# Kernel optimization log

Measured on AMD Instinct MI355X. Metric: run time of the kernel, lower is better.

The kernel has to match this reference:

```python
import jax, jax.numpy as jnp
import numpy as np

B, H, W, C, NH = 4, 128, 128, 192, 6
KD = C // NH          # key/head dim = 32
SCALING = KD ** -0.5


def dwconv5x5(v, kernel, bias):
    # v: (b,h,w,c), depthwise 5x5, stride 1, pad 2. kernel: (5,5,1,c)
    out = jax.lax.conv_general_dilated(
        v, kernel, window_strides=(1, 1), padding=[(2, 2), (2, 2)],
        dimension_numbers=("NHWC", "HWIO", "NHWC"), feature_group_count=C)
    return out + bias


def setup_inputs() -> dict:
    key = jax.random.key(0)
    ks = jax.random.split(key, 13)
    s = C ** -0.5
    return {
        "x": jax.random.normal(ks[0], (B, H, W, C), jnp.float32),
        "mask_h": 0.1 * jax.random.normal(ks[1], (1, NH, H, H), jnp.float32),
        "mask_w": 0.1 * jax.random.normal(ks[2], (1, NH, W, W), jnp.float32),
        "Wq": s * jax.random.normal(ks[3], (C, C), jnp.float32),
        "bq": 0.01 * jax.random.normal(ks[4], (C,), jnp.float32),
        "Wk": s * jax.random.normal(ks[5], (C, C), jnp.float32),
        "bk": 0.01 * jax.random.normal(ks[6], (C,), jnp.float32),
        "Wv": s * jax.random.normal(ks[7], (C, C), jnp.float32),
        "bv": 0.01 * jax.random.normal(ks[8], (C,), jnp.float32),
        "lepe_w": 0.05 * jax.random.normal(ks[9], (5, 5, 1, C), jnp.float32),
        "lepe_b": jnp.zeros((C,), jnp.float32),
        "Wo": s * jax.random.normal(ks[10], (C, C), jnp.float32),
        "bo": jnp.zeros((C,), jnp.float32),
    }


def reference(x, mask_h, mask_w, Wq, bq, Wk, bk, Wv, bv, lepe_w, lepe_b, Wo, bo):
    b, h, w, _ = x.shape
    q = x @ Wq + bq                                   # (b,h,w,c)
    k = (x @ Wk + bk) * SCALING
    v = x @ Wv + bv
    lepe = dwconv5x5(v, lepe_w, lepe_b)               # (b,h,w,c)

    qr = q.reshape(b, h, w, NH, KD)                   # (b,h,w,n,k)
    kr = k.reshape(b, h, w, NH, KD)
    vr = v.reshape(b, h, w, NH, KD)                   # head_dim == KD (factor=1)

    # ---- row (width-axis) attention ----
    # scores: (b,h,n,w,w')
    qk_w = jnp.einsum("bhwnk,bhunk->bhnwu", qr, kr)
    qk_w = qk_w + mask_w[:, None]                     # (1,1,n,w,w) broadcast over h
    attn_w = jax.nn.softmax(qk_w, axis=-1)
    v1 = jnp.einsum("bhnwu,bhund->bhnwd", attn_w, vr)  # (b,h,n,w,d)

    # ---- column (height-axis) attention ----
    # scores: (b,w,n,h,h')
    qk_h = jnp.einsum("bhwnk,bjwnk->bwnhj", qr, kr)
    qk_h = qk_h + mask_h[:, None]                     # (1,1,n,h,h) broadcast over w
    attn_h = jax.nn.softmax(qk_h, axis=-1)
    out = jnp.einsum("bwnhj,bjnwd->bhwnd", attn_h, v1)  # (b,h,w,n,d)

    out = out.reshape(b, h, w, C) + lepe
    return out @ Wo + bo
```

## Files before the change

### kernel.cpp

```cpp
#include <hip/hip_runtime.h>
#include <hip/hip_bf16.h>

#define BB  4
#define HH  128
#define WW  128
#define CC  192
#define NHH 6
#define KDD 32
#define NTOT (BB*HH*WW*CC)
#define SCALING 0.17677669529663687f
#define WMAT_ELE (12*6*64*8)

typedef __hip_bfloat16 bf16;
typedef short bf16x8 __attribute__((ext_vector_type(8)));
typedef unsigned short ushortx4 __attribute__((ext_vector_type(4)));
typedef float floatx4 __attribute__((ext_vector_type(4)));

__device__ __forceinline__ float b2f(bf16 v) { return __bfloat162float(v); }
__device__ __forceinline__ bf16  f2b(float v) { return __float2bfloat16(v); }
__device__ __forceinline__ unsigned short f2bs(float f) {
  union { bf16 b; unsigned short u; } c; c.b = __float2bfloat16(f); return c.u;
}
__device__ __forceinline__ float s2f(short s) {
  union { unsigned u; float f; } c;
  c.u = ((unsigned)(unsigned short)s) << 16; return c.f;
}

__global__ __launch_bounds__(256) void prep_kernel(
    const float* __restrict__ Wq, const float* __restrict__ Wk,
    const float* __restrict__ Wv, const float* __restrict__ Wo,
    unsigned short* __restrict__ Wt) {
  const int idx = blockIdx.x * 256 + threadIdx.x;
  if (idx >= 4 * 12 * 6 * 64) return;
  const int lane = idx & 63;
  int rest = idx >> 6;
  const int kc = rest % 6; rest /= 6;
  const int nt = rest % 12;
  const int mat = rest / 12;
  const int r16 = lane & 15, quad = lane >> 4;
  const float* W = (mat == 0) ? Wq : (mat == 1) ? Wk : (mat == 2) ? Wv : Wo;
  const float sc = (mat == 1) ? SCALING : 1.f;
  bf16x8 t;
  #pragma unroll
  for (int j = 0; j < 8; ++j)
    t[j] = (short)f2bs(W[(kc * 32 + quad * 8 + j) * CC + nt * 16 + r16] * sc);
  *reinterpret_cast<bf16x8*>(&Wt[(size_t)idx * 8]) = t;
}

__global__ __launch_bounds__(256) void qkv_mfma(
    const float* __restrict__ x, const unsigned short* __restrict__ Wt,
    const float* __restrict__ bq, const float* __restrict__ bk,
    const float* __restrict__ bv,
    bf16* __restrict__ q, bf16* __restrict__ k, bf16* __restrict__ v) {
  __shared__ __align__(16) unsigned short Wlds[18432];
  const int tid = threadIdx.x;
  const int l = tid & 63;
  const int r16 = l & 15, quad = l >> 4;
  const int row0 = blockIdx.x * 64 + (tid >> 6) * 16;
  const floatx4 zero = {0.f, 0.f, 0.f, 0.f};
  bf16x8 a[6];
  {
    const float* xrow = x + (row0 + r16) * CC;
    #pragma unroll
    for (int kc = 0; kc < 6; ++kc) {
      const float4* p = reinterpret_cast<const float4*>(xrow + kc * 32 + quad * 8);
      float4 u0 = p[0], u1 = p[1];
      bf16x8 t;
      t[0]=f2bs(u0.x); t[1]=f2bs(u0.y); t[2]=f2bs(u0.z); t[3]=f2bs(u0.w);
      t[4]=f2bs(u1.x); t[5]=f2bs(u1.y); t[6]=f2bs(u1.z); t[7]=f2bs(u1.w);
      a[kc] = t;
    }
  }
  for (int mat = 0; mat < 3; ++mat) {
    const unsigned short* Wm = Wt + mat * WMAT_ELE;
    bf16* outp = (mat == 0) ? q : (mat == 1) ? k : v;
    const float* bias = (mat == 0) ? bq : (mat == 1) ? bk : bv;
    const float bscale = (mat == 1) ? SCALING : 1.f;
    for (int hf = 0; hf < 2; ++hf) {
      __syncthreads();
      #pragma unroll
      for (int c = 0; c < 9; ++c) {
        const int ci = c * 256 + tid;
        *reinterpret_cast<bf16x8*>(&Wlds[ci * 8]) =
            *reinterpret_cast<const bf16x8*>(&Wm[hf * 18432 + ci * 8]);
      }
      __syncthreads();
      #pragma unroll
      for (int ntl = 0; ntl < 6; ++ntl) {
        const int nt = hf * 6 + ntl;
        bf16x8 wfr[6];
        #pragma unroll
        for (int kc = 0; kc < 6; ++kc)
          wfr[kc] = *reinterpret_cast<const bf16x8*>(
              &Wlds[((ntl * 6 + kc) * 64 + l) * 8]);
        floatx4 acc = zero;
        #pragma unroll
        for (int kc = 0; kc < 6; ++kc)
          acc = __builtin_amdgcn_mfma_f32_16x16x32_bf16(wfr[kc], a[kc], acc, 0, 0, 0);
        const int col0 = nt * 16 + quad * 4;
        const float4 b4 = *reinterpret_cast<const float4*>(bias + col0);
        ushortx4 s0;
        s0[0] = f2bs(acc[0] + b4.x * bscale);
        s0[1] = f2bs(acc[1] + b4.y * bscale);
        s0[2] = f2bs(acc[2] + b4.z * bscale);
        s0[3] = f2bs(acc[3] + b4.w * bscale);
        *reinterpret_cast<ushortx4*>(&outp[(row0 + r16) * CC + col0]) = s0;
      }
    }
  }
}

__global__ __launch_bounds__(256) void lepe_kernel(
    const bf16* __restrict__ v, const float* __restrict__ kw,
    const float* __restrict__ kb, float* __restrict__ lepe) {
  __shared__ __align__(16) unsigned short patch[12 * 132 * 8];
  const int tid = threadIdx.x;
  const int bid = blockIdx.x;
  const int x8 = bid & 7;
  const int kk = bid >> 3;
  const int cg = kk % 24;
  const int tile = (kk / 24) * 8 + x8;
  const int hb = tile & 15;
  const int b  = tile >> 4;
  const int c0 = cg * 8;
  const int h0 = hb * 8;
  const bf16x8 vzero = {0, 0, 0, 0, 0, 0, 0, 0};
  for (int i = tid; i < 12 * 132; i += 256) {
    const int row = i / 132, col = i % 132;
    const int gh = h0 + row - 2, gw = col - 2;
    bf16x8 t = vzero;
    if ((unsigned)gh < HH && (unsigned)gw < WW)
      t = *reinterpret_cast<const bf16x8*>(
          v + ((b * HH + gh) * WW + gw) * CC + c0);
    *reinterpret_cast<bf16x8*>(&patch[i * 8]) = t;
  }
  __syncthreads();
  const int wo = tid & 127;
  const int r0 = (tid >> 7) * 4;
  float acc[4][8];
  {
    const float4* kbp = reinterpret_cast<const float4*>(kb + c0);
    float4 b0 = kbp[0], b1 = kbp[1];
    #pragma unroll
    for (int j = 0; j < 4; ++j) {
      acc[j][0]=b0.x; acc[j][1]=b0.y; acc[j][2]=b0.z; acc[j][3]=b0.w;
      acc[j][4]=b1.x; acc[j][5]=b1.y; acc[j][6]=b1.z; acc[j][7]=b1.w;
    }
  }
  const unsigned short* pbase = &patch[(r0 * 132 + wo) * 8];
  for (int kh = 0; kh < 5; ++kh) {
    #pragma unroll
    for (int kwi = 0; kwi < 5; ++kwi) {
      const float4* kp = reinterpret_cast<const float4*>(
          kw + (kh * 5 + kwi) * CC + c0);
      float4 k0 = kp[0], k1 = kp[1];
      #pragma unroll
      for (int j = 0; j < 4; ++j) {
        bf16x8 t = *reinterpret_cast<const bf16x8*>(
            pbase + ((j + kh) * 132 + kwi) * 8);
        acc[j][0] = fmaf(s2f(t[0]), k0.x, acc[j][0]);
        acc[j][1] = fmaf(s2f(t[1]), k0.y, acc[j][1]);
        acc[j][2] = fmaf(s2f(t[2]), k0.z, acc[j][2]);
        acc[j][3] = fmaf(s2f(t[3]), k0.w, acc[j][3]);
        acc[j][4] = fmaf(s2f(t[4]), k1.x, acc[j][4]);
        acc[j][5] = fmaf(s2f(t[5]), k1.y, acc[j][5]);
        acc[j][6] = fmaf(s2f(t[6]), k1.z, acc[j][6]);
        acc[j][7] = fmaf(s2f(t[7]), k1.w, acc[j][7]);
      }
    }
  }
  #pragma unroll
  for (int j = 0; j < 4; ++j) {
    float4* op = reinterpret_cast<float4*>(
        lepe + ((b * HH + h0 + r0 + j) * WW + wo) * CC + c0);
    op[0] = make_float4(acc[j][0], acc[j][1], acc[j][2], acc[j][3]);
    op[1] = make_float4(acc[j][4], acc[j][5], acc[j][6], acc[j][7]);
  }
}

__global__ __launch_bounds__(256) void attn_mfma_kernel(
    const bf16* __restrict__ qg, const bf16* __restrict__ kg,
    bf16* vbuf, const float* __restrict__ mask,
    const float* __restrict__ lepeadd, const int rstride, const int is_col) {
  __shared__ __align__(16) unsigned short Kf[8 * 64 * 8];
  __shared__ __align__(16) unsigned short Vf[8 * 64 * 8];
  __shared__ unsigned short P[4 * 16 * 136];
  const int bid = blockIdx.x;
  const int x8 = bid & 7;
  const int kk = bid >> 3;
  const int n = kk % NHH;
  const int g = x8 * 64 + kk / NHH;
  const int p = g & 127, b = g >> 7;
  const int base = is_col ? ((b * HH * WW + p) * CC + n * KDD)
                          : (((b * HH + p) * WW) * CC + n * KDD);
  const int tid = threadIdx.x;
  const int l = tid & 63, w = tid >> 6;
  const int r16 = l & 15, quad = l >> 4;
  const float* mbase = mask + n * 128 * 128;
  const floatx4 zero = {0.f, 0.f, 0.f, 0.f};
  const unsigned short* vg = (const unsigned short*)vbuf;

  #pragma unroll
  for (int c = 0; c < 2; ++c) {
    const int chunk = c * 256 + tid;
    const int key = chunk >> 2, q4 = chunk & 3;
    const int gaddr = base + key * rstride + q4 * 8;
    bf16x8 tk = *reinterpret_cast<const bf16x8*>(kg + gaddr);
    bf16x8 tv = *reinterpret_cast<const bf16x8*>(vg + gaddr);
    *reinterpret_cast<bf16x8*>(
        &Kf[(((key >> 4) * 4 + q4) * 16 + (key & 15)) * 8]) = tk;
    const int s = key >> 5, hi = (key >> 3) & 3, j = key & 7;
    #pragma unroll
    for (int m = 0; m < 8; ++m) {
      const int ch = q4 * 8 + m;
      const int nj = ch >> 4, rr = ch & 15;
      Vf[((s * 2 + nj) * 64 + hi * 16 + rr) * 8 + j] = (unsigned short)tv[m];
    }
  }
  __syncthreads();

  unsigned short* Pw = &P[w * 2176];
  #pragma unroll
  for (int t2 = 0; t2 < 2; ++t2) {
    const int mi = w * 2 + t2;
    bf16x8 qf = *reinterpret_cast<const bf16x8*>(
        qg + base + (mi * 16 + r16) * rstride + quad * 8);
    floatx4 S[8];
    #pragma unroll
    for (int ni = 0; ni < 8; ++ni) {
      bf16x8 kfr = *reinterpret_cast<const bf16x8*>(&Kf[(ni * 64 + l) * 8]);
      S[ni] = __builtin_amdgcn_mfma_f32_16x16x32_bf16(qf, kfr, zero, 0, 0, 0);
    }
    #pragma unroll
    for (int ni = 0; ni < 8; ++ni)
      #pragma unroll
      for (int i = 0; i < 4; ++i)
        S[ni][i] += mbase[(mi * 16 + quad * 4 + i) * 128 + ni * 16 + r16];
    float linv[4], mrow[4];
    #pragma unroll
    for (int i = 0; i < 4; ++i) {
      float m = S[0][i];
      #pragma unroll
      for (int ni = 1; ni < 8; ++ni) m = fmaxf(m, S[ni][i]);
      m = fmaxf(m, __shfl_xor(m, 1));
      m = fmaxf(m, __shfl_xor(m, 2));
      m = fmaxf(m, __shfl_xor(m, 4));
      m = fmaxf(m, __shfl_xor(m, 8));
      mrow[i] = m;
    }
    #pragma unroll
    for (int i = 0; i < 4; ++i) {
      float lsum = 0.f;
      #pragma unroll
      for (int ni = 0; ni < 8; ++ni) {
        const float pv = __expf(S[ni][i] - mrow[i]);
        S[ni][i] = pv;
        lsum += pv;
      }
      lsum += __shfl_xor(lsum, 1);
      lsum += __shfl_xor(lsum, 2);
      lsum += __shfl_xor(lsum, 4);
      lsum += __shfl_xor(lsum, 8);
      linv[i] = 1.f / lsum;
    }
    #pragma unroll
    for (int ni = 0; ni < 8; ++ni)
      #pragma unroll
      for (int i = 0; i < 4; ++i)
        Pw[(quad * 4 + i) * 136 + ni * 16 + r16] = f2bs(S[ni][i] * linv[i]);
    floatx4 O[2] = {zero, zero};
    #pragma unroll
    for (int s = 0; s < 4; ++s) {
      bf16x8 pf = *reinterpret_cast<const bf16x8*>(
          &Pw[r16 * 136 + s * 32 + quad * 8]);
      #pragma unroll
      for (int nj = 0; nj < 2; ++nj) {
        bf16x8 vfr = *reinterpret_cast<const bf16x8*>(
            &Vf[((s * 2 + nj) * 64 + l) * 8]);
        O[nj] = __builtin_amdgcn_mfma_f32_16x16x32_bf16(pf, vfr, O[nj], 0, 0, 0);
      }
    }
    #pragma unroll
    for (int nj = 0; nj < 2; ++nj)
      #pragma unroll
      for (int i = 0; i < 4; ++i) {
        const int addr = base + (mi * 16 + quad * 4 + i) * rstride + nj * 16 + r16;
        float val = O[nj][i];
        if (lepeadd) val += lepeadd[addr];
        vbuf[addr] = f2b(val);
      }
  }
}

__global__ __launch_bounds__(256) void proj_mfma(
    const bf16* __restrict__ pre, const unsigned short* __restrict__ Wto,
    const float* __restrict__ bo, float* __restrict__ out) {
  __shared__ __align__(16) unsigned short Wlds[18432];
  const int tid = threadIdx.x;
  const int l = tid & 63;
  const int r16 = l & 15, quad = l >> 4;
  const int row0 = blockIdx.x * 128 + (tid >> 6) * 32;
  const floatx4 zero = {0.f, 0.f, 0.f, 0.f};
  bf16x8 a[2][6];
  #pragma unroll
  for (int rs = 0; rs < 2; ++rs)
    #pragma unroll
    for (int kc = 0; kc < 6; ++kc)
      a[rs][kc] = *reinterpret_cast<const bf16x8*>(
          pre + (row0 + rs * 16 + r16) * CC + kc * 32 + quad * 8);
  for (int hf = 0; hf < 2; ++hf) {
    __syncthreads();
    #pragma unroll
    for (int c = 0; c < 9; ++c) {
      const int ci = c * 256 + tid;
      *reinterpret_cast<bf16x8*>(&Wlds[ci * 8]) =
          *reinterpret_cast<const bf16x8*>(&Wto[hf * 18432 + ci * 8]);
    }
    __syncthreads();
    #pragma unroll
    for (int ntl = 0; ntl < 6; ++ntl) {
      const int nt = hf * 6 + ntl;
      bf16x8 wfr[6];
      #pragma unroll
      for (int kc = 0; kc < 6; ++kc)
        wfr[kc] = *reinterpret_cast<const bf16x8*>(
            &Wlds[((ntl * 6 + kc) * 64 + l) * 8]);
      floatx4 acc0 = zero, acc1 = zero;
      #pragma unroll
      for (int kc = 0; kc < 6; ++kc) {
        acc0 = __builtin_amdgcn_mfma_f32_16x16x32_bf16(wfr[kc], a[0][kc], acc0, 0, 0, 0);
        acc1 = __builtin_amdgcn_mfma_f32_16x16x32_bf16(wfr[kc], a[1][kc], acc1, 0, 0, 0);
      }
      const int col0 = nt * 16 + quad * 4;
      const float4 b4 = *reinterpret_cast<const float4*>(bo + col0);
      float4 s0 = make_float4(acc0[0] + b4.x, acc0[1] + b4.y,
                              acc0[2] + b4.z, acc0[3] + b4.w);
      float4 s1 = make_float4(acc1[0] + b4.x, acc1[1] + b4.y,
                              acc1[2] + b4.z, acc1[3] + b4.w);
      *reinterpret_cast<float4*>(&out[(row0 + r16) * CC + col0]) = s0;
      *reinterpret_cast<float4*>(&out[(row0 + 16 + r16) * CC + col0]) = s1;
    }
  }
}

extern "C" void kernel_launch(void* const* d_in, const int* in_sizes, int n_in,
                              void* d_out, int out_size, void* d_ws, size_t ws_size,
                              hipStream_t stream) {
  const float* x      = (const float*)d_in[0];
  const float* mask_h = (const float*)d_in[1];
  const float* mask_w = (const float*)d_in[2];
  const float* Wq = (const float*)d_in[3];
  const float* bq = (const float*)d_in[4];
  const float* Wk = (const float*)d_in[5];
  const float* bk = (const float*)d_in[6];
  const float* Wv = (const float*)d_in[7];
  const float* bv = (const float*)d_in[8];
  const float* lw = (const float*)d_in[9];
  const float* lb = (const float*)d_in[10];
  const float* Wo = (const float*)d_in[11];
  const float* bo = (const float*)d_in[12];
  float* out = (float*)d_out;

  bf16* q    = (bf16*)d_ws;
  bf16* kbuf = q + NTOT;
  bf16* v    = kbuf + NTOT;
  unsigned short* Wt = (unsigned short*)(v + NTOT);

  prep_kernel<<<(4*12*6*64 + 255)/256, 256, 0, stream>>>(Wq, Wk, Wv, Wo, Wt);
  qkv_mfma<<<(BB*HH*WW)/64, 256, 0, stream>>>(x, Wt, bq, bk, bv, q, kbuf, v);
  lepe_kernel<<<BB*16*24, 256, 0, stream>>>(v, lw, lb, out);
  attn_mfma_kernel<<<BB*128*NHH, 256, 0, stream>>>(
      q, kbuf, v, mask_w, nullptr, CC, 0);
  attn_mfma_kernel<<<BB*128*NHH, 256, 0, stream>>>(
      q, kbuf, v, mask_h, out, WW*CC, 1);
  proj_mfma<<<(BB*HH*WW)/128, 256, 0, stream>>>(v, Wt + 3*WMAT_ELE, bo, out);
}
```

Before: 276.4 us.

## Double-buffer QKV weight staging with async global-to-LDS loads

The QKV projection kernel now stages weight tiles through two LDS buffers using direct global_load_lds instructions, prefetching the next quarter-matrix while computing the current one. Weight phases are split into 12 smaller chunks instead of 6 halves, so LDS use stays the same but the load no longer passes through registers or sits on the critical path. This depends on the async LDS load finishing before the __syncthreads barrier without an explicit vmcnt wait, which is a correctness risk. The QKV kernel is only part of the total pipeline time.

```diff
diff --git a/kernel.cpp b/kernel.cpp
--- a/kernel.cpp
+++ b/kernel.cpp
@@ -24,6 +24,13 @@
 __device__ __forceinline__ float s2f(short s) {
   union { unsigned u; float f; } c;
   c.u = ((unsigned)(unsigned short)s) << 16; return c.f;
+}
+
+__device__ __forceinline__ void stage16(const unsigned short* g,
+                                        unsigned short* l) {
+  __builtin_amdgcn_global_load_lds(
+      (const __attribute__((address_space(1))) void*)g,
+      (__attribute__((address_space(3))) void*)l, 16, 0, 0);
 }
 
 __global__ __launch_bounds__(256) void prep_kernel(
@@ -52,11 +59,11 @@
     const float* __restrict__ bq, const float* __restrict__ bk,
     const float* __restrict__ bv,
     bf16* __restrict__ q, bf16* __restrict__ k, bf16* __restrict__ v) {
-  __shared__ __align__(16) unsigned short Wlds[18432];
+  __shared__ __align__(16) unsigned short Wlds[2][9216];
   const int tid = threadIdx.x;
-  const int l = tid & 63;
+  const int l = tid & 63, w = tid >> 6;
   const int r16 = l & 15, quad = l >> 4;
-  const int row0 = blockIdx.x * 64 + (tid >> 6) * 16;
+  const int row0 = blockIdx.x * 64 + w * 16;
   const floatx4 zero = {0.f, 0.f, 0.f, 0.f};
   bf16x8 a[6];
   {
@@ -71,43 +78,46 @@
       a[kc] = t;
     }
   }
-  for (int mat = 0; mat < 3; ++mat) {
-    const unsigned short* Wm = Wt + mat * WMAT_ELE;
+  #define STAGE_Q(ph, dst)                                                \
+    {                                                                     \
+      const unsigned short* src_ =                                        \
+          Wt + ((ph) >> 2) * WMAT_ELE + ((ph) & 3) * 9216;                \
+      for (int seg = w; seg < 18; seg += 4)                               \
+        stage16(src_ + seg * 512 + l * 8, &dst[seg * 512]);               \
+    }
+  STAGE_Q(0, Wlds[0]);
+  __syncthreads();
+  for (int ph = 0; ph < 12; ++ph) {
+    const int cur = ph & 1;
+    if (ph < 11) STAGE_Q(ph + 1, Wlds[cur ^ 1]);
+    const int mat = ph >> 2, qq = ph & 3;
     bf16* outp = (mat == 0) ? q : (mat == 1) ? k : v;
     const float* bias = (mat == 0) ? bq : (mat == 1) ? bk : bv;
     const float bscale = (mat == 1) ? SCALING : 1.f;
-    for (int hf = 0; hf < 2; ++hf) {
-      __syncthreads();
-      #pragma unroll
-      for (int c = 0; c < 9; ++c) {
-        const int ci = c * 256 + tid;
-        *reinterpret_cast<bf16x8*>(&Wlds[ci * 8]) =
-            *reinterpret_cast<const bf16x8*>(&Wm[hf * 18432 + ci * 8]);
-      }
-      __syncthreads();
-      #pragma unroll
-      for (int ntl = 0; ntl < 6; ++ntl) {
-        const int nt = hf * 6 + ntl;
-        bf16x8 wfr[6];
-        #pragma unroll
-        for (int kc = 0; kc < 6; ++kc)
-          wfr[kc] = *reinterpret_cast<const bf16x8*>(
-              &Wlds[((ntl * 6 + kc) * 64 + l) * 8]);
-        floatx4 acc = zero;
-        #pragma unroll
-        for (int kc = 0; kc < 6; ++kc)
-          acc = __builtin_amdgcn_mfma_f32_16x16x32_bf16(wfr[kc], a[kc], acc, 0, 0, 0);
-        const int col0 = nt * 16 + quad * 4;
-        const float4 b4 = *reinterpret_cast<const float4*>(bias + col0);
-        ushortx4 s0;
-        s0[0] = f2bs(acc[0] + b4.x * bscale);
-        s0[1] = f2bs(acc[1] + b4.y * bscale);
-        s0[2] = f2bs(acc[2] + b4.z * bscale);
-        s0[3] = f2bs(acc[3] + b4.w * bscale);
-        *reinterpret_cast<ushortx4*>(&outp[(row0 + r16) * CC + col0]) = s0;
-      }
-    }
-  }
+    #pragma unroll
+    for (int ntl = 0; ntl < 3; ++ntl) {
+      const int nt = qq * 3 + ntl;
+      bf16x8 wfr[6];
+      #pragma unroll
+      for (int kc = 0; kc < 6; ++kc)
+        wfr[kc] = *reinterpret_cast<const bf16x8*>(
+            &Wlds[cur][(ntl * 6 + kc) * 512 + l * 8]);
+      floatx4 acc = zero;
+      #pragma unroll
+      for (int kc = 0; kc < 6; ++kc)
+        acc = __builtin_amdgcn_mfma_f32_16x16x32_bf16(wfr[kc], a[kc], acc, 0, 0, 0);
+      const int col0 = nt * 16 + quad * 4;
+      const float4 b4 = *reinterpret_cast<const float4*>(bias + col0);
+      ushortx4 s0;
+      s0[0] = f2bs(acc[0] + b4.x * bscale);
+      s0[1] = f2bs(acc[1] + b4.y * bscale);
+      s0[2] = f2bs(acc[2] + b4.z * bscale);
+      s0[3] = f2bs(acc[3] + b4.w * bscale);
+      *reinterpret_cast<ushortx4*>(&outp[(row0 + r16) * CC + col0]) = s0;
+    }
+    __syncthreads();
+  }
+  #undef STAGE_Q
 }
 
 __global__ __launch_bounds__(256) void lepe_kernel(
```

Measured after the change: 275.3 us. About the same (-0.4%).
